# Optimization experiments

Measured on AMD Instinct MI355X. Metric: run time of the kernel, lower is better.

Reference implementation:

```python
import jax, jax.numpy as jnp
import numpy as np

HEADS = 16
DK = 64
THETA = 10000.0


def _rope(x, cos, sin):
    # x: (B, S, H, dk) -> rotate consecutive pairs as complex numbers
    xr = x.reshape(*x.shape[:-1], -1, 2)
    a, b = xr[..., 0], xr[..., 1]
    c = cos[None, :, None, :]  # (1, S, 1, dk//2)
    s = sin[None, :, None, :]
    out = jnp.stack([a * c - b * s, a * s + b * c], axis=-1)
    return out.reshape(x.shape)


def setup_inputs() -> dict:
    key = jax.random.key(0)
    ks = jax.random.split(key, 5)
    B, S, D = 4, 2048, 1024
    x = jax.random.normal(ks[0], (B, S, D), dtype=jnp.float32)
    scale = 1.0 / np.sqrt(D).astype(np.float32)
    Wq = jax.random.normal(ks[1], (D, D), dtype=jnp.float32) * scale
    Wk = jax.random.normal(ks[2], (D, D), dtype=jnp.float32) * scale
    Wv = jax.random.normal(ks[3], (D, D), dtype=jnp.float32) * scale
    Wo = jax.random.normal(ks[4], (D, D), dtype=jnp.float32) * scale
    # freqs_cis = exp(i * t * theta^{-2j/dk}), represented as cos/sin
    t = jnp.arange(S, dtype=jnp.float32)
    inv_freq = 1.0 / (THETA ** (jnp.arange(0, DK, 2, dtype=jnp.float32) / DK))
    ang = t[:, None] * inv_freq[None, :]  # (S, dk//2)
    return {"in_features": x, "freqs_cos": jnp.cos(ang), "freqs_sin": jnp.sin(ang),
            "Wq": Wq, "Wk": Wk, "Wv": Wv, "Wo": Wo}


def reference(in_features, freqs_cos, freqs_sin, Wq, Wk, Wv, Wo):
    B, S, D = in_features.shape
    H = HEADS
    dk = D // H
    # Linear projections (torch Linear: x @ W.T)
    q = (in_features @ Wq.T).reshape(B, S, H, dk)
    k = (in_features @ Wk.T).reshape(B, S, H, dk)
    v = (in_features @ Wv.T).reshape(B, S, H, dk)
    q = _rope(q, freqs_cos, freqs_sin)
    k = _rope(k, freqs_cos, freqs_sin)
    scale = 1.0 / jnp.sqrt(jnp.asarray(dk, dtype=q.dtype))
    scores = jnp.einsum("bqhd,bkhd->bhqk", q, k) * scale
    mask = jnp.tril(jnp.ones((S, S), dtype=bool))
    scores = jnp.where(mask[None, None, :, :], scores, -jnp.inf)
    attn = jax.nn.softmax(scores, axis=-1)
    out = jnp.einsum("bhqk,bkhd->bqhd", attn, v).reshape(B, S, D)
    return out @ Wo.T
```

## Files before the change

### kernel.cpp

```cpp
#include <hip/hip_runtime.h>
#include <hip/hip_bf16.h>

typedef __attribute__((ext_vector_type(8))) __bf16 bf16x8;
typedef __attribute__((ext_vector_type(4))) __bf16 bf16x4;
typedef __attribute__((ext_vector_type(4))) float f32x4;
typedef __attribute__((ext_vector_type(2))) unsigned int u32x2;

static __device__ __forceinline__ f32x4 mfma_bf16(bf16x8 a, bf16x8 b, f32x4 c) {
  return __builtin_amdgcn_mfma_f32_16x16x32_bf16(a, b, c, 0, 0, 0);
}

static __device__ __forceinline__ void gload_lds16(const void* g, void* l) {
  __builtin_amdgcn_global_load_lds(
      (__attribute__((address_space(1))) unsigned int*)g,
      (__attribute__((address_space(3))) unsigned int*)l, 16, 0, 0);
}

static __device__ __forceinline__ unsigned int pk_bf16(float a, float b) {
  union { __bf16 h; unsigned short u; } x, y;
  x.h = (__bf16)a; y.h = (__bf16)b;
  return ((unsigned int)y.u << 16) | x.u;
}

__global__ void cvt_bf16(const float* __restrict__ in, __bf16* __restrict__ out, int n4) {
  int i = blockIdx.x * blockDim.x + threadIdx.x;
  if (i >= n4) return;
  f32x4 v = ((const f32x4*)in)[i];
  bf16x4 o;
#pragma unroll
  for (int k = 0; k < 4; ++k) o[k] = (__bf16)v[k];
  ((bf16x4*)out)[i] = o;
}

__global__ void cvt_w4(const float* __restrict__ w0, const float* __restrict__ w1,
                       const float* __restrict__ w2, const float* __restrict__ w3,
                       __bf16* __restrict__ o0, __bf16* __restrict__ o1,
                       __bf16* __restrict__ o2, __bf16* __restrict__ o3) {
  const float* in; __bf16* out;
  switch (blockIdx.y) {
    case 0: in = w0; out = o0; break;
    case 1: in = w1; out = o1; break;
    case 2: in = w2; out = o2; break;
    default: in = w3; out = o3; break;
  }
  int i = blockIdx.x * blockDim.x + threadIdx.x;
  f32x4 v = ((const f32x4*)in)[i];
  bf16x4 o;
#pragma unroll
  for (int k = 0; k < 4; ++k) o[k] = (__bf16)v[k];
  ((bf16x4*)out)[i] = o;
}

template <int MODE>
__global__ __launch_bounds__(512, 1)
void gemm256(const __bf16* __restrict__ A, const __bf16* __restrict__ W,
             void* __restrict__ outp,
             const float* __restrict__ fcos, const float* __restrict__ fsin) {
  constexpr int K = 1024;
  constexpr int NT = K / 64;
  extern __shared__ __align__(16) __bf16 dynlds[];
  __bf16* Al = dynlds;
  __bf16* Bl = dynlds + 49152;

  const int t = threadIdx.x;
  const int lane = t & 63, wave = t >> 6;
  const int g = lane >> 4, ln = lane & 15;
  const int wm = wave >> 1, wn = wave & 1;
  const int bn = blockIdx.x, bm = blockIdx.y;

  f32x4 acc[4][4] = {};

  const int srow8 = t >> 3;
  const int scole = (((t & 7) ^ ((t >> 3) & 7)) << 3);
  const __bf16* Ag = A + (size_t)(bm * 256 + srow8) * K + scole;
  const __bf16* Wg = W + (size_t)(bn * 128 + srow8) * K + scole;

#define ISSUE_A(kt, slot)                                                   \
  {                                                                         \
    const int k0 = (kt) * 64;                                               \
    __bf16* d = Al + (slot) * 16384 + t * 8;                                \
    gload_lds16(Ag + k0, d);                                                \
    gload_lds16(Ag + (size_t)64 * K + k0, d + 4096);                        \
    gload_lds16(Ag + (size_t)128 * K + k0, d + 8192);                       \
    gload_lds16(Ag + (size_t)192 * K + k0, d + 12288);                      \
  }
#define ISSUE_B(kt, slot)                                                   \
  {                                                                         \
    const int k0 = (kt) * 64;                                               \
    __bf16* d = Bl + (slot) * 8192 + t * 8;                                 \
    gload_lds16(Wg + k0, d);                                                \
    gload_lds16(Wg + (size_t)64 * K + k0, d + 4096);                        \
  }

  const int axr = ln & 7;
  int aoff[4], boff[4];
#pragma unroll
  for (int i = 0; i < 4; ++i) aoff[i] = (wm * 64 + i * 16 + ln) * 64;
#pragma unroll
  for (int j = 0; j < 4; ++j) boff[j] = (wn * 64 + j * 16 + ln) * 64;

  ISSUE_B(0, 0);
  ISSUE_A(0, 0);
  ISSUE_A(1, 1);
  asm volatile("s_waitcnt vmcnt(4)" ::: "memory");
  __builtin_amdgcn_s_barrier();

  int sa = 0;
  for (int tt = 0; tt < NT; ++tt) {
    const __bf16* Ab = Al + sa * 16384;
    const __bf16* Bb = Bl + (tt & 1) * 8192;
    bf16x8 af[4], bf[4];

#pragma unroll
    for (int i = 0; i < 4; ++i)
      af[i] = *(const bf16x8*)(Ab + aoff[i] + ((g ^ axr) << 3));
#pragma unroll
    for (int j = 0; j < 4; ++j)
      bf[j] = *(const bf16x8*)(Bb + boff[j] + ((g ^ axr) << 3));
    if (tt + 1 < NT) ISSUE_B(tt + 1, (tt + 1) & 1);
    if (tt + 2 < NT) ISSUE_A(tt + 2, sa == 0 ? 2 : sa - 1);
    __builtin_amdgcn_s_barrier();
    asm volatile("s_waitcnt lgkmcnt(0)" ::: "memory");
    __builtin_amdgcn_sched_barrier(0);
    __builtin_amdgcn_s_setprio(1);
#pragma unroll
    for (int i = 0; i < 4; ++i)
#pragma unroll
      for (int j = 0; j < 4; ++j)
        acc[i][j] = mfma_bf16(af[i], bf[j], acc[i][j]);
    __builtin_amdgcn_s_setprio(0);
    __builtin_amdgcn_s_barrier();

#pragma unroll
    for (int i = 0; i < 4; ++i)
      af[i] = *(const bf16x8*)(Ab + aoff[i] + (((4 | g) ^ axr) << 3));
#pragma unroll
    for (int j = 0; j < 4; ++j)
      bf[j] = *(const bf16x8*)(Bb + boff[j] + (((4 | g) ^ axr) << 3));
    if (tt < NT - 2) { asm volatile("s_waitcnt vmcnt(4)" ::: "memory"); }
    else             { asm volatile("s_waitcnt vmcnt(0)" ::: "memory"); }
    __builtin_amdgcn_s_barrier();
    asm volatile("s_waitcnt lgkmcnt(0)" ::: "memory");
    __builtin_amdgcn_sched_barrier(0);
    __builtin_amdgcn_s_setprio(1);
#pragma unroll
    for (int i = 0; i < 4; ++i)
#pragma unroll
      for (int j = 0; j < 4; ++j)
        acc[i][j] = mfma_bf16(af[i], bf[j], acc[i][j]);
    __builtin_amdgcn_s_setprio(0);
    __builtin_amdgcn_s_barrier();

    sa = (sa == 2) ? 0 : sa + 1;
  }
#undef ISSUE_A
#undef ISSUE_B

#pragma unroll
  for (int i = 0; i < 4; ++i) {
    const int mbase = bm * 256 + wm * 64 + i * 16 + g * 4;
#pragma unroll
    for (int j = 0; j < 4; ++j) {
      const int col = bn * 128 + wn * 64 + j * 16 + ln;
      if constexpr (MODE == 0 || MODE == 1) {
        const int fi = (col & 63) >> 1;
        const bool odd = (col & 1) != 0;
        __bf16* O = (__bf16*)outp;
#pragma unroll
        for (int r = 0; r < 4; ++r) {
          const int row = mbase + r;
          const int tok = row & 2047;
          const float cs = fcos[tok * 32 + fi];
          const float sn = fsin[tok * 32 + fi];
          const float own = acc[i][j][r];
          const float oth = __shfl_xor(own, 1);
          float val = own * cs + (odd ? oth * sn : -oth * sn);
          if constexpr (MODE == 0) val *= 0.1803368802f;
          O[(size_t)row * 1024 + col] = (__bf16)val;
        }
      } else if constexpr (MODE == 2) {
        __bf16* O = (__bf16*)outp;
        const int bb = mbase >> 11;
        const int tok = mbase & 2047;
        bf16x4 pk;
#pragma unroll
        for (int r = 0; r < 4; ++r) pk[r] = (__bf16)acc[i][j][r];
        *(bf16x4*)(O + ((size_t)(bb * 1024 + col)) * 2048 + tok) = pk;
      } else {
        float* O = (float*)outp;
#pragma unroll
        for (int r = 0; r < 4; ++r)
          O[(size_t)(mbase + r) * 1024 + col] = acc[i][j][r];
      }
    }
  }
}

__global__ __launch_bounds__(512, 4)
void attn_fwd(const __bf16* __restrict__ Q, const __bf16* __restrict__ Kk,
              const __bf16* __restrict__ Vt, __bf16* __restrict__ U) {
  constexpr int S = 2048;
  __shared__ __align__(16) __bf16 Klds[2][2 * 64 * 32];
  __shared__ __align__(16) __bf16 Vlds[2][2 * 64 * 32];
  __shared__ __align__(16) unsigned int Plds[8][16 * 36];

  const int t = threadIdx.x;
  const int lane = t & 63, wave = t >> 6;
  const int g = lane >> 4, ln = lane & 15;
  const int qt = blockIdx.x;
  const int bh = blockIdx.y;
  const int b = bh >> 4, h = bh & 15;
  const int q0s[2] = {qt * 128, (15 - qt) * 128};
  const int nts[2] = {2 * qt + 2, 32 - 2 * qt};

  bf16x8 qf[2][2];
#pragma unroll
  for (int s2 = 0; s2 < 2; ++s2) {
    const __bf16* Qb = Q + ((size_t)(b * S + q0s[s2] + wave * 16 + ln)) * 1024 + h * 64;
    qf[s2][0] = *(const bf16x8*)(Qb + g * 8);
    qf[s2][1] = *(const bf16x8*)(Qb + 32 + g * 8);
  }

  f32x4 o[2][4] = {};
  float mrow[2], lrow[2];
#pragma unroll
  for (int s2 = 0; s2 < 2; ++s2) { mrow[s2] = -3.0e38f; lrow[s2] = 0.f; }

  const int half = t >> 8;
  const int srow = (t >> 2) & 63;
  const int scol = (t & 3) * 8;
  const __bf16* Kg = Kk + ((size_t)(b * S + srow)) * 1024 + h * 64 + half * 32 + scol;
  const __bf16* Vg = Vt + ((size_t)(b * 1024 + h * 64 + srow)) * 2048 + half * 32 + scol;
  const int nt = nts[1];

  gload_lds16(Kg, (__bf16*)Klds[0] + t * 8);
  gload_lds16(Vg, (__bf16*)Vlds[0] + t * 8);
  __syncthreads();

  for (int kt = 0; kt < nt; ++kt) {
    const int cur = kt & 1;
    if (kt + 1 < nt) {
      const size_t kv1 = (size_t)(kt + 1) * 64;
      gload_lds16(Kg + kv1 * 1024, (__bf16*)Klds[cur ^ 1] + t * 8);
      gload_lds16(Vg + kv1, (__bf16*)Vlds[cur ^ 1] + t * 8);
    }
    const int kv0 = kt * 64;

#pragma unroll
    for (int s2 = 0; s2 < 2; ++s2) {
      if (kt >= nts[s2]) continue;

      f32x4 sa[4] = {};
      __builtin_amdgcn_s_setprio(1);
#pragma unroll
      for (int s = 0; s < 2; ++s) {
#pragma unroll
        for (int c = 0; c < 4; ++c) {
          bf16x8 kf = *(const bf16x8*)(Klds[cur] + s * 2048 + (c * 16 + ln) * 32 + g * 8);
          sa[c] = mfma_bf16(kf, qf[s2][s], sa[c]);
        }
      }
      __builtin_amdgcn_s_setprio(0);

      const int rfbase = q0s[s2] + wave * 16;
      const int rq = rfbase + ln;
      if (kv0 + 63 > rfbase) {
#pragma unroll
        for (int c = 0; c < 4; ++c)
#pragma unroll
          for (int r = 0; r < 4; ++r)
            if (kv0 + c * 16 + g * 4 + r > rq) sa[c][r] = -1e30f;
      }

      float tm[8];
#pragma unroll
      for (int i = 0; i < 8; ++i) tm[i] = fmaxf(sa[i >> 2][i & 3], sa[2 + (i >> 2)][i & 3]);
#pragma unroll
      for (int st = 4; st >= 1; st >>= 1)
#pragma unroll
        for (int i = 0; i < st; ++i) tm[i] = fmaxf(tm[i], tm[i + st]);
      float pm = tm[0];

      if (__any(pm > mrow[s2] + 8.f)) {
        pm = fmaxf(pm, __shfl_xor(pm, 16));
        pm = fmaxf(pm, __shfl_xor(pm, 32));
        const float mn = fmaxf(mrow[s2], pm);
        const float alpha = exp2f(mrow[s2] - mn);
        mrow[s2] = mn;
        lrow[s2] *= alpha;
#pragma unroll
        for (int c2 = 0; c2 < 4; ++c2)
#pragma unroll
          for (int r = 0; r < 4; ++r) o[s2][c2][r] *= alpha;
      }

      float p[4][4];
#pragma unroll
      for (int c = 0; c < 4; ++c)
#pragma unroll
        for (int r = 0; r < 4; ++r) p[c][r] = exp2f(sa[c][r] - mrow[s2]);

      float ts[8];
#pragma unroll
      for (int i = 0; i < 8; ++i) ts[i] = p[i >> 2][i & 3] + p[2 + (i >> 2)][i & 3];
#pragma unroll
      for (int st = 4; st >= 1; st >>= 1)
#pragma unroll
        for (int i = 0; i < st; ++i) ts[i] += ts[i + st];
      float rs = ts[0];
      rs += __shfl_xor(rs, 16);
      rs += __shfl_xor(rs, 32);
      lrow[s2] += rs;

      unsigned int* Pw = Plds[wave] + ln * 36;
#pragma unroll
      for (int c = 0; c < 4; ++c) {
        u32x2 w;
        w[0] = pk_bf16(p[c][0], p[c][1]);
        w[1] = pk_bf16(p[c][2], p[c][3]);
        *(u32x2*)(Pw + 8 * c + 2 * g) = w;
      }

      __builtin_amdgcn_s_setprio(1);
#pragma unroll
      for (int sh = 0; sh < 2; ++sh) {
        bf16x8 pb = *(const bf16x8*)((const __bf16*)(Plds[wave]) + ln * 72 + sh * 32 + g * 8);
#pragma unroll
        for (int c2 = 0; c2 < 4; ++c2) {
          bf16x8 vf = *(const bf16x8*)(Vlds[cur] + sh * 2048 + (c2 * 16 + ln) * 32 + g * 8);
          o[s2][c2] = mfma_bf16(vf, pb, o[s2][c2]);
        }
      }
      __builtin_amdgcn_s_setprio(0);
    }
    __syncthreads();
  }

#pragma unroll
  for (int s2 = 0; s2 < 2; ++s2) {
    const float rl = 1.0f / lrow[s2];
    __bf16* Ub = U + ((size_t)(b * S + q0s[s2] + wave * 16 + ln)) * 1024 + h * 64;
#pragma unroll
    for (int c2 = 0; c2 < 4; ++c2) {
      bf16x4 pk4;
#pragma unroll
      for (int r = 0; r < 4; ++r) pk4[r] = (__bf16)(o[s2][c2][r] * rl);
      *(bf16x4*)(Ub + 16 * c2 + 4 * g) = pk4;
    }
  }
}

extern "C" void kernel_launch(void* const* d_in, const int* in_sizes, int n_in,
                              void* d_out, int out_size, void* d_ws, size_t ws_size,
                              hipStream_t stream) {
  const float* x    = (const float*)d_in[0];
  const float* fcos = (const float*)d_in[1];
  const float* fsin = (const float*)d_in[2];
  const float* Wq   = (const float*)d_in[3];
  const float* Wk   = (const float*)d_in[4];
  const float* Wv   = (const float*)d_in[5];
  const float* Wo   = (const float*)d_in[6];

  char* ws = (char*)d_ws;
  __bf16* xb  = (__bf16*)(ws);
  __bf16* Wqb = (__bf16*)(ws + (16u << 20));
  __bf16* Wkb = (__bf16*)(ws + (18u << 20));
  __bf16* Wvb = (__bf16*)(ws + (20u << 20));
  __bf16* Wob = (__bf16*)(ws + (22u << 20));
  __bf16* Qb  = (__bf16*)(ws + (24u << 20));
  __bf16* Kb  = (__bf16*)(ws + (40u << 20));
  __bf16* Vtb = (__bf16*)(ws + (56u << 20));
  __bf16* Ub  = xb;

  cvt_bf16<<<8192, 256, 0, stream>>>(x, xb, 8192 * 1024 / 4);
  cvt_w4<<<dim3(1024, 4), 256, 0, stream>>>(Wq, Wk, Wv, Wo, Wqb, Wkb, Wvb, Wob);

  dim3 gg(8, 32);
  const size_t lds = 131072;
  gemm256<0><<<gg, 512, lds, stream>>>(xb, Wqb, Qb,  fcos, fsin);
  gemm256<1><<<gg, 512, lds, stream>>>(xb, Wkb, Kb,  fcos, fsin);
  gemm256<2><<<gg, 512, lds, stream>>>(xb, Wvb, Vtb, nullptr, nullptr);
  attn_fwd<<<dim3(8, 64), 512, 0, stream>>>(Qb, Kb, Vtb, Ub);
  gemm256<3><<<gg, 512, lds, stream>>>(Ub, Wob, d_out, nullptr, nullptr);
}
```

Measured before the change: 210.5 us.

## Swizzle block order for L2 locality, use packed bf16 convert, restructure max

Remaps the linear block index in the GEMM and attention kernels so that neighbouring workgroups share weight/row tiles and batch-heads differently, aiming for better L2/cache reuse across concurrently scheduled blocks. Replaces the union-based bf16 packing of softmax probabilities with the hardware v_cvt_pk_bf16_f32 instruction via inline asm. Rewrites the row-max reduction as a tree of three-input fmax calls so it can map to v_max3. The grid remapping assumes specific grid dimensions; if the launch shapes differ, the mapping could be wrong.

```diff
diff --git a/kernel.cpp b/kernel.cpp
--- a/kernel.cpp
+++ b/kernel.cpp
@@ -16,10 +16,10 @@
       (__attribute__((address_space(3))) unsigned int*)l, 16, 0, 0);
 }
 
-static __device__ __forceinline__ unsigned int pk_bf16(float a, float b) {
-  union { __bf16 h; unsigned short u; } x, y;
-  x.h = (__bf16)a; y.h = (__bf16)b;
-  return ((unsigned int)y.u << 16) | x.u;
+static __device__ __forceinline__ unsigned int cvt_pk_bf16(float lo, float hi) {
+  unsigned int r;
+  asm volatile("v_cvt_pk_bf16_f32 %0, %1, %2" : "=v"(r) : "v"(lo), "v"(hi));
+  return r;
 }
 
 __global__ void cvt_bf16(const float* __restrict__ in, __bf16* __restrict__ out, int n4) {
@@ -66,7 +66,9 @@
   const int lane = t & 63, wave = t >> 6;
   const int g = lane >> 4, ln = lane & 15;
   const int wm = wave >> 1, wn = wave & 1;
-  const int bn = blockIdx.x, bm = blockIdx.y;
+  const int lin = blockIdx.x + blockIdx.y * 8;
+  const int bm = (lin & 7) + 8 * ((lin >> 3) & 3);
+  const int bn = lin >> 5;
 
   f32x4 acc[4][4] = {};
 
@@ -207,8 +209,9 @@
   const int t = threadIdx.x;
   const int lane = t & 63, wave = t >> 6;
   const int g = lane >> 4, ln = lane & 15;
-  const int qt = blockIdx.x;
-  const int bh = blockIdx.y;
+  const int lin = blockIdx.x + blockIdx.y * 8;
+  const int bh = (lin & 7) * 8 + ((lin >> 3) & 7);
+  const int qt = lin >> 6;
   const int b = bh >> 4, h = bh & 15;
   const int q0s[2] = {qt * 128, (15 - qt) * 128};
   const int nts[2] = {2 * qt + 2, 32 - 2 * qt};
@@ -272,14 +275,14 @@
             if (kv0 + c * 16 + g * 4 + r > rq) sa[c][r] = -1e30f;
       }
 
-      float tm[8];
-#pragma unroll
-      for (int i = 0; i < 8; ++i) tm[i] = fmaxf(sa[i >> 2][i & 3], sa[2 + (i >> 2)][i & 3]);
-#pragma unroll
-      for (int st = 4; st >= 1; st >>= 1)
-#pragma unroll
-        for (int i = 0; i < st; ++i) tm[i] = fmaxf(tm[i], tm[i + st]);
-      float pm = tm[0];
+      const float a0 = fmaxf(fmaxf(sa[0][0], sa[0][1]), sa[0][2]);
+      const float a1 = fmaxf(fmaxf(sa[0][3], sa[1][0]), sa[1][1]);
+      const float a2 = fmaxf(fmaxf(sa[1][2], sa[1][3]), sa[2][0]);
+      const float a3 = fmaxf(fmaxf(sa[2][1], sa[2][2]), sa[2][3]);
+      const float a4 = fmaxf(fmaxf(sa[3][0], sa[3][1]), sa[3][2]);
+      const float b0 = fmaxf(fmaxf(a0, a1), a2);
+      const float b1 = fmaxf(fmaxf(a3, a4), sa[3][3]);
+      float pm = fmaxf(b0, b1);
 
       if (__any(pm > mrow[s2] + 8.f)) {
         pm = fmaxf(pm, __shfl_xor(pm, 16));
@@ -316,8 +319,8 @@
 #pragma unroll
       for (int c = 0; c < 4; ++c) {
         u32x2 w;
-        w[0] = pk_bf16(p[c][0], p[c][1]);
-        w[1] = pk_bf16(p[c][2], p[c][3]);
+        w[0] = cvt_pk_bf16(p[c][0], p[c][1]);
+        w[1] = cvt_pk_bf16(p[c][2], p[c][3]);
         *(u32x2*)(Pw + 8 * c + 2 * g) = w;
       }
 
```

After: 187.3 us. -11.0%, faster.
